# Kernel tuning notes

Hardware: AMD Instinct MI355X
Metric: run time of the kernel (lower is better)

The kernel has to match this reference:

```python
import jax, jax.numpy as jnp
import numpy as np

B, N, D, J, L = 8, 2046, 128, 128, 2  # batch, ops, feature len, jobs, blocks
C = N + 2  # ops + appended begin/end rows


def setup_inputs() -> dict:
    key = jax.random.key(0)
    ks = jax.random.split(key, 40)

    def w(k, shape, fan_in):
        return jax.random.normal(k, shape, jnp.float32) / np.float32(np.sqrt(fan_in))

    inp = {}
    inp["operation_features"] = jax.random.normal(ks[0], (B, N, D), jnp.float32)
    inp["same_type_mask"] = (jax.random.uniform(ks[1], (B, N, N)) > 0.5).astype(jnp.float32)
    inp["relations"] = jax.random.randint(ks[2], (B, N, 2), 0, N, jnp.int32)
    inp["begins_idx"] = jax.random.randint(ks[3], (B, J), 0, N, jnp.int32)
    inp["ends_idx"] = jax.random.randint(ks[4], (B, J), 0, N, jnp.int32)
    # begin_end_init params
    inp["init_bp_w"] = w(ks[5], (D, D), D); inp["init_bp_b"] = jnp.zeros((D,), jnp.float32)
    inp["init_ep_w"] = w(ks[6], (D, D), D); inp["init_ep_b"] = jnp.zeros((D,), jnp.float32)
    # per-block params, stacked on leading L axis
    inp["be_bp_w"] = w(ks[7], (L, D, D), D); inp["be_bp_b"] = jnp.zeros((L, D), jnp.float32)
    inp["be_ep_w"] = w(ks[8], (L, D, D), D); inp["be_ep_b"] = jnp.zeros((L, D), jnp.float32)
    inp["seq_mix_w"] = w(ks[9], (L, 3 * D, D), 3 * D); inp["seq_mix_b"] = jnp.zeros((L, D), jnp.float32)
    inp["attn_w_w"] = w(ks[10], (L, D, 3 * D), D); inp["attn_w_b"] = jnp.zeros((L, 3 * D), jnp.float32)
    inp["score_w"] = w(ks[11], (L, 2 * D), 2 * D); inp["score_b"] = jnp.zeros((L,), jnp.float32)
    inp["attn_out_w"] = w(ks[12], (L, D, D), D); inp["attn_out_b"] = jnp.zeros((L, D), jnp.float32)
    inp["mix_w"] = w(ks[13], (L, 2 * D, D), 2 * D); inp["mix_b"] = jnp.zeros((L, D), jnp.float32)
    return inp


def _begin_end(ops, begins_idx, ends_idx, bp_w, bp_b, ep_w, ep_b):
    gb = jnp.take_along_axis(ops, begins_idx[..., None], axis=1)  # [B,J,D]
    ge = jnp.take_along_axis(ops, ends_idx[..., None], axis=1)
    begin = jnp.mean(gb @ bp_w + bp_b, axis=1)  # [B,D]
    end = jnp.mean(ge @ ep_w + ep_b, axis=1)
    return begin, end


def _forward(operation_features, same_type_mask,
             init_bp_w, init_bp_b, init_ep_w, init_ep_b,
             be_bp_w, be_bp_b, be_ep_w, be_ep_b,
             seq_mix_w, seq_mix_b, attn_w_w, attn_w_b,
             score_w, score_b, attn_out_w, attn_out_b,
             mix_w, mix_b, relations, begins_idx, ends_idx):
    begin, end = _begin_end(operation_features, begins_idx, ends_idx,
                            init_bp_w, init_bp_b, init_ep_w, init_ep_b)
    feats = jnp.concatenate([operation_features, begin[:, None], end[:, None]], axis=1)  # [B,C,D]
    # -1 sentinels point to appended begin/end rows
    rel_p = jnp.where(relations[..., 0] == -1, N, relations[..., 0])  # [B,N]
    rel_s = jnp.where(relations[..., 1] == -1, N + 1, relations[..., 1])
    mask = jnp.zeros((B, C, C), jnp.float32)
    mask = mask.at[:, :N, :N].set(same_type_mask)
    mask = mask.at[:, N, N].set(1.0).at[:, N + 1, N + 1].set(1.0)

    for l in range(L):
        # --- OperationTimeRelationEncoder ---
        pred = jnp.take_along_axis(feats, rel_p[..., None], axis=1)  # [B,N,D]
        succ = jnp.take_along_axis(feats, rel_s[..., None], axis=1)
        mixed = jnp.concatenate([feats[:, :N], pred, succ], axis=-1) @ seq_mix_w[l] + seq_mix_b[l]
        b2, e2 = _begin_end(feats, begins_idx, ends_idx,
                            be_bp_w[l], be_bp_b[l], be_ep_w[l], be_ep_b[l])
        seq_feats = jnp.concatenate([mixed, b2[:, None], e2[:, None]], axis=1)  # [B,C,D]
        # --- SelfAttention (GAT-style concat score) ---
        qkv = feats @ attn_w_w[l] + attn_w_b[l]
        q, k, v = jnp.split(qkv, 3, axis=-1)  # each [B,C,D]
        wq, wk = score_w[l][:D], score_w[l][D:]
        # score(concat(q_i, k_j)) = q_i.wq + k_j.wk + b, then LeakyReLU
        scores = jax.nn.leaky_relu((q @ wq)[:, :, None] + (k @ wk)[:, None, :] + score_b[l])  # [B,C,C]
        attn = jax.nn.softmax(scores * mask, axis=-1)
        weighted = jnp.einsum('bij,bjh->bih', attn, v)  # [B,C,D]
        attn_out = weighted @ attn_out_w[l] + attn_out_b[l]
        # --- block mix ---
        feats = jnp.concatenate([seq_feats, attn_out], axis=-1) @ mix_w[l] + mix_b[l]

    return jnp.mean(feats, axis=1), feats


def reference(operation_features, same_type_mask,
              init_bp_w, init_bp_b, init_ep_w, init_ep_b,
              be_bp_w, be_bp_b, be_ep_w, be_ep_b,
              seq_mix_w, seq_mix_b, attn_w_w, attn_w_b,
              score_w, score_b, attn_out_w, attn_out_b,
              mix_w, mix_b, relations, begins_idx, ends_idx):
    return _forward(operation_features, same_type_mask,
                    init_bp_w, init_bp_b, init_ep_w, init_ep_b,
                    be_bp_w, be_bp_b, be_ep_w, be_ep_b,
                    seq_mix_w, seq_mix_b, attn_w_w, attn_w_b,
                    score_w, score_b, attn_out_w, attn_out_b,
                    mix_w, mix_b, relations, begins_idx, ends_idx)
```

## Files before the change

### kernel.cpp

```cpp
#include <hip/hip_runtime.h>

constexpr int kB = 8;
constexpr int kN = 2046;
constexpr int kC = 2048;
constexpr int kD = 128;
constexpr int kJ = 128;
constexpr int kL = 2;

typedef short bfrag8 __attribute__((ext_vector_type(8)));
typedef float f32x4 __attribute__((ext_vector_type(4)));

__device__ __forceinline__ float bf2f(unsigned short h) {
  union { unsigned u; float f; } x; x.u = ((unsigned)h) << 16; return x.f;
}
__device__ __forceinline__ unsigned short f2bf(float f) {
  union { float f; unsigned u; } x; x.f = f;
  unsigned u = x.u;
  if ((u & 0x7fffffffu) > 0x7f800000u) return (unsigned short)((u >> 16) | 0x40);
  return (unsigned short)((u + 0x7fffu + ((u >> 16) & 1u)) >> 16);
}
__device__ __forceinline__ unsigned short f2bf_fast(float f) {
  union { float f; unsigned u; } x; x.f = f;
  return (unsigned short)((x.u + 0x7fffu + ((x.u >> 16) & 1u)) >> 16);
}
__device__ __forceinline__ void split2(float x, unsigned short& h, unsigned short& l) {
  unsigned short hh = f2bf_fast(x);
  h = hh;
  l = f2bf_fast(x - bf2f(hh));
}

struct Raw {
  const void *ops, *mask;
  const int *rel, *bidx, *eidx;
  const void *ibw, *ibb, *iew, *ieb;
  const void *bbw, *bbb, *bew, *beb;
  const void *sw, *sb;
  const void *aw, *ab;
  const void *scw, *scb;
  const void *aow, *aob;
  const void *mw, *mb;
};

__device__ __forceinline__ float rp(const void* p, size_t i, bool bf) {
  return bf ? bf2f(((const unsigned short*)p)[i]) : ((const float*)p)[i];
}

__device__ __forceinline__ bool sniff(const Raw& r) {
  const unsigned* x = (const unsigned*)r.ops;
  int lane = (int)(threadIdx.x & 63);
  int hits = 0;
  #pragma unroll
  for (int q = 0; q < 16; ++q) {
    unsigned w = x[q * 64 + lane];
    unsigned e0 = (w >> 7) & 0xFFu;
    hits += (e0 == 0u || (e0 >= 96u && e0 <= 134u)) ? 1 : 0;
  }
  #pragma unroll
  for (int o = 1; o < 64; o <<= 1) hits += __shfl_xor(hits, o);
  return hits >= 512;
}

constexpr size_t OF_FEATS = 0;
constexpr size_t OF_SEQ   = 2097152;
constexpr size_t OF_ATTN  = 4194304;
constexpr size_t OF_V     = 6291456;
constexpr size_t OF_SQ    = 8388608;
constexpr size_t OF_SK    = 8404992;
constexpr size_t OF_U     = 8421376;
constexpr size_t OF_PART  = 8422400;
constexpr size_t OF_BMIX  = 8423424;
constexpr size_t OF_WT    = 8423680;

constexpr int WT_SEQH = 0;
constexpr int WT_SEQL = 49152;
constexpr int WT_VH   = 98304;
constexpr int WT_VL   = 114688;
constexpr int WT_MIXH = 131072;
constexpr int WT_MIXL = 163840;
constexpr int WT_LS   = 196608;

constexpr int RP_CAST = 4092;
constexpr int RP_MASK = 8184;
constexpr int RP_WT   = 8824;
constexpr int RP_WF   = 9082;
constexpr int RP_UV   = 9084;
constexpr int RP_BE   = 9100;
constexpr int RP_TOT  = 9101;

__device__ __forceinline__ f32x4 mfma16(bfrag8 a, bfrag8 b, f32x4 c) {
  return __builtin_amdgcn_mfma_f32_16x16x32_bf16(a, b, c, 0, 0, 0);
}

__global__ __launch_bounds__(256) void k_prep(Raw r, float* __restrict__ feats,
                                              unsigned* __restrict__ bits32,
                                              unsigned short* __restrict__ wt,
                                              float* __restrict__ bmix,
                                              float* __restrict__ u2,
                                              float* __restrict__ part) {
  __shared__ __align__(16) char smem[4096];
  int bid = blockIdx.x, t = threadIdx.x;
  bool bf = sniff(r);

  if (bid < RP_CAST) {
    int idx = bid * 256 + t;
    int elem = idx * 2;
    int b = elem / (kN * kD);
    int rr = elem - b * (kN * kD);
    float2 f;
    if (bf) {
      unsigned u = ((const unsigned*)r.ops)[idx];
      f.x = bf2f((unsigned short)(u & 0xffffu));
      f.y = bf2f((unsigned short)(u >> 16));
    } else {
      f = ((const float2*)r.ops)[idx];
    }
    *(float2*)(feats + (size_t)b * kC * kD + rr) = f;
  } else if (bid < RP_MASK) {
    int wave = t >> 6, lane = t & 63;
    int rr = (bid - RP_CAST) * 4 + wave;
    int b = rr / kN, i = rr - b * kN;
    unsigned chunk = 0;
    int je0 = lane * 32;
    if (bf) {
      const unsigned short* mrow = (const unsigned short*)r.mask + (size_t)rr * kN;
      if (je0 + 32 <= kN) {
        const unsigned* p32 = (const unsigned*)mrow;
        #pragma unroll
        for (int g = 0; g < 16; ++g) {
          unsigned v = p32[lane * 16 + g];
          if (v & 0xFFFFu) chunk |= 1u << (g * 2);
          if (v >> 16)     chunk |= 1u << (g * 2 + 1);
        }
      } else {
        for (int jj = je0; jj < kN; ++jj)
          if (mrow[jj] != 0) chunk |= 1u << (jj - je0);
      }
    } else {
      const unsigned* mrow = (const unsigned*)r.mask + (size_t)rr * kN;
      if (je0 + 32 <= kN) {
        const uint2* p64 = (const uint2*)mrow;
        #pragma unroll
        for (int g = 0; g < 16; ++g) {
          uint2 v = p64[lane * 16 + g];
          if (v.x) chunk |= 1u << (g * 2);
          if (v.y) chunk |= 1u << (g * 2 + 1);
        }
      } else {
        for (int jj = je0; jj < kN; ++jj)
          if (mrow[jj] != 0) chunk |= 1u << (jj - je0);
      }
    }
    bits32[((size_t)b * kC + i) * 64 + lane] = chunk;
  } else if (bid < RP_WT) {
    int idx = (bid - RP_MASK) * 256 + t;
    int l = idx / 81920;
    int rr = idx - l * 81920;
    const void* src; size_t si; int dH, dL, k, n;
    if (rr < 49152) {
      k = rr >> 7; n = rr & 127;
      src = r.sw; si = (size_t)l * 49152 + (size_t)k * 128 + n;
      dH = l * WT_LS + WT_SEQH; dL = l * WT_LS + WT_SEQL;
    } else if (rr < 65536) {
      int e = rr - 49152; k = e >> 7; n = e & 127;
      src = r.aw; si = (size_t)l * 49152 + (size_t)k * 384 + 256 + n;
      dH = l * WT_LS + WT_VH; dL = l * WT_LS + WT_VL;
    } else {
      int e = rr - 65536; k = e >> 7; n = e & 127;
      src = r.mw; si = (size_t)l * 32768 + (size_t)k * 128 + n;
      dH = l * WT_LS + WT_MIXH; dL = l * WT_LS + WT_MIXL;
    }
    float v = rp(src, si, bf);
    unsigned short h, lo;
    split2(v, h, lo);
    int kc = k >> 5, q = (k >> 3) & 3, e8 = k & 7;
    int fa = ((kc * 8 + (n >> 4)) * 64 + (q * 16 + (n & 15))) * 8 + e8;
    wt[dH + fa] = h;
    wt[dL + fa] = lo;
  } else if (bid < RP_WF) {
    int rb = bid - RP_WT;
    int l = rb / 129, d1 = rb - l * 129;
    if (t < 128) {
      int d = t;
      size_t mixbot = (size_t)l * 32768 + 16384;
      if (d1 < 128) {
        float acc = 0.f;
        for (int d2 = 0; d2 < kD; ++d2)
          acc += rp(r.aow, (size_t)l * 16384 + (size_t)d1 * 128 + d2, bf)
               * rp(r.mw, mixbot + (size_t)d2 * 128 + d, bf);
        unsigned short h, lo;
        split2(acc, h, lo);
        int k = 128 + d1;
        int kc = k >> 5, q = (k >> 3) & 3, e8 = k & 7;
        int fa = ((kc * 8 + (d >> 4)) * 64 + (q * 16 + (d & 15))) * 8 + e8;
        wt[l * WT_LS + WT_MIXH + fa] = h;
        wt[l * WT_LS + WT_MIXL + fa] = lo;
      } else {
        float acc = rp(r.mb, (size_t)l * 128 + d, bf);
        for (int d2 = 0; d2 < kD; ++d2)
          acc += rp(r.aob, (size_t)l * 128 + d2, bf)
               * rp(r.mw, mixbot + (size_t)d2 * 128 + d, bf);
        bmix[(size_t)l * kD + d] = acc;
      }
    }
  } else if (bid < RP_UV) {
    int l = bid - RP_WF;
    float* swm = (float*)smem;
    float* red = (float*)smem + 256;
    if (t < 128) {
      swm[t]       = rp(r.scw, (size_t)l * 256 + t, bf);
      swm[128 + t] = rp(r.scw, (size_t)l * 256 + 128 + t, bf);
    }
    __syncthreads();
    if (t < 128) {
      int k = t;
      size_t base = (size_t)l * 49152 + (size_t)k * 384;
      float uq = 0.f, uk = 0.f;
      for (int d2 = 0; d2 < kD; ++d2) {
        uq += rp(r.aw, base + d2, bf) * swm[d2];
        uk += rp(r.aw, base + 128 + d2, bf) * swm[128 + d2];
      }
      float* u = u2 + (size_t)l * 272;
      u[k] = uq; u[128 + k] = uk;
      red[k] = rp(r.ab, (size_t)l * 384 + k, bf) * swm[k]
             + rp(r.ab, (size_t)l * 384 + 128 + k, bf) * swm[128 + k];
    }
    __syncthreads();
    if (t == 0) {
      float s = rp(r.scb, l, bf);
      for (int i = 0; i < 128; ++i) s += red[i];
      u2[(size_t)l * 272 + 256] = s;
    }
  } else if (bid < RP_BE) {
    int rb = bid - RP_UV;
    int b = rb >> 1, sel = rb & 1;
    float* msh = (float*)smem;
    const int* idx = (sel ? r.eidx : r.bidx) + b * kJ;
    const void* wv = sel ? r.iew : r.ibw;
    const void* bb = sel ? r.ieb : r.ibb;
    if (t < 128) {
      int d = t;
      float acc = 0.f;
      for (int j = 0; j < kJ; ++j)
        acc += rp(r.ops, ((size_t)b * kN + idx[j]) * kD + d, bf);
      msh[d] = acc * (1.0f / kJ);
    }
    __syncthreads();
    if (t < 128) {
      int d = t;
      float o = rp(bb, d, bf);
      for (int k = 0; k < kD; ++k) o += msh[k] * rp(wv, (size_t)k * kD + d, bf);
      feats[(size_t)b * kC * kD + (size_t)(kN + sel) * kD + d] = o;
    }
  } else {
    #pragma unroll
    for (int q = 0; q < 4; ++q) part[q * 256 + t] = 0.f;
  }
}

__global__ __launch_bounds__(256) void k_stage1(Raw r, int l,
    const float* __restrict__ feats, const unsigned short* __restrict__ wt,
    const float* __restrict__ u2, float* __restrict__ seq,
    unsigned short* __restrict__ Vt, float* __restrict__ sq, float* __restrict__ sk)
{
  __shared__ __align__(16) char smem[21504];
  unsigned short (*Ah)[64 * 40] = (unsigned short(*)[64 * 40])smem;
  unsigned short (*Al)[64 * 40] = (unsigned short(*)[64 * 40])(smem + 10240);
  float* su = (float*)(smem + 20480);
  int bid = blockIdx.x, t = threadIdx.x;
  int lane = t & 63, w = t >> 6, m = lane & 15, quad = lane >> 4;
  bool bf = sniff(r);
  const unsigned short* wl = wt + (size_t)l * WT_LS;

  if (bid < 512) {
    bool isv = bid >= 256;
    int rb = isv ? bid - 256 : bid;
    int gr0 = rb * 64;
    int b = gr0 >> 11, r0 = gr0 & 2047;
    int arow = t >> 2, kq = (t & 3) * 8;
    int nl = r0 + arow;
    const float* fb = feats + (size_t)b * kC * kD;
    const float *s0, *s1, *s2;
    if (!isv) {
      int nr = (nl <= kN - 1) ? nl : (kN - 1);
      const int* rel = r.rel + ((size_t)b * kN + nr) * 2;
      int rpd = rel[0], rsc = rel[1];
      int p = (rpd < 0) ? kN : rpd;
      int s = (rsc < 0) ? (kN + 1) : rsc;
      s0 = fb + (size_t)nl * kD;
      s1 = fb + (size_t)p * kD;
      s2 = fb + (size_t)s * kD;
    } else {
      s0 = fb + (size_t)nl * kD; s1 = s0; s2 = s0;
      su[t] = u2[(size_t)l * 272 + t];
    }
    const int K = isv ? 128 : 384;
    const unsigned short* wth = isv ? (wl + WT_VH) : (wl + WT_SEQH);
    const unsigned short* wtl = isv ? (wl + WT_VL) : (wl + WT_SEQL);
    const unsigned short* pbh = wth + (size_t)(w * 2) * 512 + lane * 8;
    const unsigned short* pbl = wtl + (size_t)(w * 2) * 512 + lane * 8;
    float pq = 0.f, pk2 = 0.f;

    auto build = [&](int kb, int buf) {
      int kg = kb + kq;
      const float* sp;
      if (!isv) sp = (kg < 128) ? (s0 + kg) : (kg < 256) ? (s1 + kg - 128) : (s2 + kg - 256);
      else      sp = s0 + kg;
      float4 xa = *(const float4*)sp;
      float4 xb = *(const float4*)(sp + 4);
      if (isv) {
        pq  += xa.x * su[kg]     + xa.y * su[kg + 1] + xa.z * su[kg + 2] + xa.w * su[kg + 3]
             + xb.x * su[kg + 4] + xb.y * su[kg + 5] + xb.z * su[kg + 6] + xb.w * su[kg + 7];
        pk2 += xa.x * su[128 + kg]     + xa.y * su[128 + kg + 1] + xa.z * su[128 + kg + 2] + xa.w * su[128 + kg + 3]
             + xb.x * su[128 + kg + 4] + xb.y * su[128 + kg + 5] + xb.z * su[128 + kg + 6] + xb.w * su[128 + kg + 7];
      }
      unsigned short h[8], lo[8];
      split2(xa.x, h[0], lo[0]); split2(xa.y, h[1], lo[1]);
      split2(xa.z, h[2], lo[2]); split2(xa.w, h[3], lo[3]);
      split2(xb.x, h[4], lo[4]); split2(xb.y, h[5], lo[5]);
      split2(xb.z, h[6], lo[6]); split2(xb.w, h[7], lo[7]);
      uint4 ph, pl;
      ph.x = h[0] | ((unsigned)h[1] << 16);  ph.y = h[2] | ((unsigned)h[3] << 16);
      ph.z = h[4] | ((unsigned)h[5] << 16);  ph.w = h[6] | ((unsigned)h[7] << 16);
      pl.x = lo[0] | ((unsigned)lo[1] << 16); pl.y = lo[2] | ((unsigned)lo[3] << 16);
      pl.z = lo[4] | ((unsigned)lo[5] << 16); pl.w = lo[6] | ((unsigned)lo[7] << 16);
      *(uint4*)&Ah[buf][arow * 40 + kq] = ph;
      *(uint4*)&Al[buf][arow * 40 + kq] = pl;
    };

    f32x4 acc[4][2];
    #pragma unroll
    for (int mi = 0; mi < 4; ++mi) { acc[mi][0] = {0.f,0.f,0.f,0.f}; acc[mi][1] = {0.f,0.f,0.f,0.f}; }

    __syncthreads();
    build(0, 0);
    __syncthreads();
    for (int kb = 0; kb < K; kb += 32) {
      int cur = (kb >> 5) & 1;
      int kc = kb >> 5;
      bfrag8 bh0 = *(const bfrag8*)(pbh + (size_t)kc * 4096);
      bfrag8 bh1 = *(const bfrag8*)(pbh + (size_t)kc * 4096 + 512);
      bfrag8 bl0 = {}, bl1 = {};
      if (!bf) {
        bl0 = *(const bfrag8*)(pbl + (size_t)kc * 4096);
        bl1 = *(const bfrag8*)(pbl + (size_t)kc * 4096 + 512);
      }
      if (kb + 32 < K) build(kb + 32, cur ^ 1);
      #pragma unroll
      for (int mi = 0; mi < 4; ++mi) {
        bfrag8 ah = *(const bfrag8*)&Ah[cur][(mi * 16 + m) * 40 + quad * 8];
        bfrag8 al = *(const bfrag8*)&Al[cur][(mi * 16 + m) * 40 + quad * 8];
        acc[mi][0] = mfma16(ah, bh0, acc[mi][0]);
        acc[mi][0] = mfma16(al, bh0, acc[mi][0]);
        acc[mi][1] = mfma16(ah, bh1, acc[mi][1]);
        acc[mi][1] = mfma16(al, bh1, acc[mi][1]);
        if (!bf) {
          acc[mi][0] = mfma16(ah, bl0, acc[mi][0]);
          acc[mi][1] = mfma16(ah, bl1, acc[mi][1]);
        }
      }
      __syncthreads();
    }

    int n0 = w * 32 + m;
    if (!isv) {
      float bv0 = rp(r.sb, (size_t)l * 128 + n0, bf);
      float bv1 = rp(r.sb, (size_t)l * 128 + n0 + 16, bf);
      #pragma unroll
      for (int mi = 0; mi < 4; ++mi)
        #pragma unroll
        for (int reg = 0; reg < 4; ++reg) {
          int ra = r0 + mi * 16 + quad * 4 + reg;
          if (ra < kN) {
            seq[((size_t)b * kC + ra) * kD + n0]      = acc[mi][0][reg] + bv0;
            seq[((size_t)b * kC + ra) * kD + n0 + 16] = acc[mi][1][reg] + bv1;
          }
        }
    } else {
      float bv0 = rp(r.ab, (size_t)l * 384 + 256 + n0, bf);
      float bv1 = rp(r.ab, (size_t)l * 384 + 256 + n0 + 16, bf);
      unsigned short* vtb = Vt + (size_t)b * 262144;
      #pragma unroll
      for (int mi = 0; mi < 4; ++mi)
        #pragma unroll
        for (int reg = 0; reg < 4; ++reg) {
          int c = r0 + mi * 16 + quad * 4 + reg;
          int kc = c >> 5, cq = (c >> 3) & 3, e8 = c & 7;
          int lp = cq * 16 + m;
          vtb[((kc * 8 + w * 2) * 64 + lp) * 8 + e8]       = f2bf_fast(acc[mi][0][reg] + bv0);
          vtb[((kc * 8 + w * 2 + 1) * 64 + lp) * 8 + e8]   = f2bf_fast(acc[mi][1][reg] + bv1);
        }
      pq  += __shfl_xor(pq, 1);  pq  += __shfl_xor(pq, 2);
      pk2 += __shfl_xor(pk2, 1); pk2 += __shfl_xor(pk2, 2);
      if ((t & 3) == 0) {
        sq[(size_t)b * kC + nl] = pq + u2[(size_t)l * 272 + 256];
        sk[(size_t)b * kC + nl] = pk2;
      }
    }
  } else {
    int rb = bid - 512;
    int b = rb >> 1, sel = rb & 1;
    float* msh = (float*)smem;
    const int* idx = (sel ? r.eidx : r.bidx) + b * kJ;
    const void* wv = sel ? r.bew : r.bbw;
    const void* bb = sel ? r.beb : r.bbb;
    size_t wbase = (size_t)l * kD * kD, bbase = (size_t)l * kD;
    if (t < 128) {
      int d = t;
      const float* fb2 = feats + (size_t)b * kC * kD;
      float acc = 0.f;
      for (int j = 0; j < kJ; ++j) acc += fb2[(size_t)idx[j] * kD + d];
      msh[d] = acc * (1.0f / kJ);
    }
    __syncthreads();
    if (t < 128) {
      int d = t;
      float o = rp(bb, bbase + d, bf);
      for (int k = 0; k < kD; ++k) o += msh[k] * rp(wv, wbase + (size_t)k * kD + d, bf);
      seq[(size_t)b * kC * kD + (size_t)(kN + sel) * kD + d] = o;
    }
  }
}

__global__ __launch_bounds__(256) void k_attn_pv_mfma(
    const unsigned* __restrict__ bits,
    const float* __restrict__ sq, const float* __restrict__ sk,
    const unsigned short* __restrict__ Vt,
    float* __restrict__ outw)
{
  int b = blockIdx.y;
  int i0 = blockIdx.x * 32;
  int t = threadIdx.x, lane = t & 63, w = t >> 6;

  __shared__ unsigned short pshare[2][1024];
  __shared__ float sklds[kC];
  __shared__ unsigned bitlds[2048];
  __shared__ float ssq[32], smx[32], szv[32];

  const float* skb = sk + (size_t)b * kC;
  #pragma unroll
  for (int q = 0; q < 8; ++q) sklds[q * 256 + t] = skb[q * 256 + t];
  const unsigned* bitrow = bits + ((size_t)b * kC + i0) * 64;
  #pragma unroll
  for (int q = 0; q < 8; ++q) bitlds[q * 256 + t] = bitrow[q * 256 + t];
  if (t < 32) ssq[t] = sq[(size_t)b * kC + i0 + t];
  __syncthreads();

  {
    int rr = t >> 3, seg = t & 7;
    int ig = i0 + rr;
    bool ok = (ig < kN);
    float sqi2 = ssq[rr];
    const unsigned* bw = bitlds + rr * 64 + seg * 8;
    const float* sks = sklds + seg * 256;
    float mx;
    if (ok) {
      float msk = -3e38f;
      #pragma unroll 1
      for (int w8 = 0; w8 < 8; ++w8) {
        unsigned bb = bw[w8];
        #pragma unroll
        for (int q4 = 0; q4 < 8; ++q4) {
          float4 skv = *(const float4*)(sks + w8 * 32 + q4 * 4);
          unsigned nib = bb >> (q4 * 4);
          msk = (nib & 1u) ? fmaxf(msk, skv.x) : msk;
          msk = (nib & 2u) ? fmaxf(msk, skv.y) : msk;
          msk = (nib & 4u) ? fmaxf(msk, skv.z) : msk;
          msk = (nib & 8u) ? fmaxf(msk, skv.w) : msk;
        }
      }
      #pragma unroll
      for (int d2 = 1; d2 < 8; d2 <<= 1) msk = fmaxf(msk, __shfl_xor(msk, d2));
      float s = sqi2 + msk;
      mx = fmaxf(0.f, fmaxf(s, 0.01f * s));
    } else {
      float s = sqi2 + sklds[ig & (kC - 1)];
      mx = fmaxf(0.f, fmaxf(s, 0.01f * s));
    }
    float emx = __expf(-mx);
    float zs = 0.f;
    if (ok) {
      #pragma unroll 1
      for (int w8 = 0; w8 < 8; ++w8) {
        unsigned bb = bw[w8];
        #pragma unroll
        for (int q4 = 0; q4 < 8; ++q4) {
          float4 skv = *(const float4*)(sks + w8 * 32 + q4 * 4);
          unsigned nib = bb >> (q4 * 4);
          float s1 = sqi2 + skv.x, l1 = fmaxf(s1, 0.01f * s1);
          float s2 = sqi2 + skv.y, l2 = fmaxf(s2, 0.01f * s2);
          float s3 = sqi2 + skv.z, l3 = fmaxf(s3, 0.01f * s3);
          float s4 = sqi2 + skv.w, l4 = fmaxf(s4, 0.01f * s4);
          zs += (nib & 1u) ? __expf(l1 - mx) : emx;
          zs += (nib & 2u) ? __expf(l2 - mx) : emx;
          zs += (nib & 4u) ? __expf(l3 - mx) : emx;
          zs += (nib & 8u) ? __expf(l4 - mx) : emx;
        }
      }
    } else {
      zs = 256.f * emx;
      if ((ig >> 8) == seg) {
        float s = sqi2 + sklds[ig & (kC - 1)];
        float lr = fmaxf(s, 0.01f * s);
        zs += __expf(lr - mx) - emx;
      }
    }
    #pragma unroll
    for (int d2 = 1; d2 < 8; d2 <<= 1) zs += __shfl_xor(zs, d2);
    if (seg == 0) { smx[rr] = mx; szv[rr] = 1.0f / zs; }
  }
  __syncthreads();

  int f = t >> 1, h = t & 1;
  int mt_b = f >> 6;
  int lb = f & 63;
  int irow_l = mt_b * 16 + (lb & 15);
  int quad_b = lb >> 4;
  int i_g = i0 + irow_l;
  float sqi = ssq[irow_l];
  float mri = smx[irow_l];
  int joff = quad_b * 8 + h * 4;
  bool irow_ok = (i_g < kN);
  const unsigned char* bitb = (const unsigned char*)bitlds + irow_l * 256;

  auto buildP = [&](int k0, int buf) {
    float4 skv = *(const float4*)(sklds + k0 + joff);
    unsigned byte;
    if (irow_ok) {
      byte = bitb[(k0 >> 3) + quad_b];
    } else {
      int d0 = i_g - (k0 + quad_b * 8);
      byte = ((unsigned)d0 < 8u) ? (1u << d0) : 0u;
    }
    unsigned nib = byte >> (h * 4);
    unsigned short us[4];
    float sv[4] = {skv.x, skv.y, skv.z, skv.w};
    #pragma unroll
    for (int dj = 0; dj < 4; ++dj) {
      float s = sqi + sv[dj];
      float lr = fmaxf(s, 0.01f * s);
      float val = ((nib >> dj) & 1u) ? lr : 0.f;
      us[dj] = f2bf_fast(__expf(val - mri));
    }
    uint2 pk;
    pk.x = us[0] | ((unsigned)us[1] << 16);
    pk.y = us[2] | ((unsigned)us[3] << 16);
    *(uint2*)(&pshare[buf][f * 8 + h * 4]) = pk;
  };

  f32x4 acc00 = {0.f, 0.f, 0.f, 0.f}, acc01 = acc00, acc10 = acc00, acc11 = acc00;
  int m = lane & 15, quad = lane >> 4;
  int nbase = w * 32;
  const unsigned short* vtb = Vt + (size_t)b * 262144;
  const unsigned short* p0 = vtb + (size_t)(w * 2) * 512 + lane * 8;
  const unsigned short* p1 = p0 + 512;

  buildP(0, 0);
  bfrag8 b0n = *(const bfrag8*)p0;
  bfrag8 b1n = *(const bfrag8*)p1;
  __syncthreads();

  for (int k0 = 0; k0 < kC; k0 += 32) {
    int cur = (k0 >> 5) & 1;
    bfrag8 bf0 = b0n, bf1 = b1n;
    if (k0 + 32 < kC) {
      size_t off = (size_t)((k0 >> 5) + 1) * 4096;
      b0n = *(const bfrag8*)(p0 + off);
      b1n = *(const bfrag8*)(p1 + off);
    }
    bfrag8 a0 = *(const bfrag8*)(&pshare[cur][(0 * 64 + lane) * 8]);
    bfrag8 a1 = *(const bfrag8*)(&pshare[cur][(1 * 64 + lane) * 8]);
    acc00 = mfma16(a0, bf0, acc00);
    acc01 = mfma16(a0, bf1, acc01);
    acc10 = mfma16(a1, bf0, acc10);
    acc11 = mfma16(a1, bf1, acc11);
    if (k0 + 32 < kC) buildP(k0 + 32, cur ^ 1);
    __syncthreads();
  }

  #pragma unroll
  for (int reg = 0; reg < 4; ++reg) {
    int il_a = quad * 4 + reg;
    int i_a = i0 + il_a;
    int i_b = i_a + 16;
    float za = szv[il_a];
    float zb = szv[il_a + 16];
    float* oa = outw + ((size_t)b * kC + i_a) * kD + nbase + m;
    float* ob = outw + ((size_t)b * kC + i_b) * kD + nbase + m;
    oa[0]  = acc00[reg] * za;
    oa[16] = acc01[reg] * za;
    ob[0]  = acc10[reg] * zb;
    ob[16] = acc11[reg] * zb;
  }
}

__global__ __launch_bounds__(256) void k_mix64(Raw r, int l,
    const float* __restrict__ seqb, const float* __restrict__ attnw,
    const unsigned short* __restrict__ wt, const float* __restrict__ bmix,
    float* __restrict__ featsOut, void* __restrict__ outx, float* __restrict__ part,
    int mode)
{
  __shared__ __align__(16) char smem[20480];
  unsigned short (*Ah)[64 * 40] = (unsigned short(*)[64 * 40])smem;
  unsigned short (*Al)[64 * 40] = (unsigned short(*)[64 * 40])(smem + 10240);
  constexpr int K = 256;
  int bid = blockIdx.x, t = threadIdx.x;
  int lane = t & 63, w = t >> 6, m = lane & 15, quad = lane >> 4;
  bool bf = sniff(r);
  int gr0 = bid * 64;
  int b = gr0 >> 11;
  int arow = t >> 2, kq = (t & 3) * 8;
  const float* s0 = seqb  + (size_t)(gr0 + arow) * kD;
  const float* s1 = attnw + (size_t)(gr0 + arow) * kD;
  const unsigned short* wth = wt + (size_t)l * WT_LS + WT_MIXH;
  const unsigned short* wtl = wt + (size_t)l * WT_LS + WT_MIXL;
  const unsigned short* pbh = wth + (size_t)(w * 2) * 512 + lane * 8;
  const unsigned short* pbl = wtl + (size_t)(w * 2) * 512 + lane * 8;

  auto build = [&](int kb, int buf) {
    int kg = kb + kq;
    const float* sp = (kg < kD) ? (s0 + kg) : (s1 + kg - kD);
    float4 xa = *(const float4*)sp;
    float4 xb = *(const float4*)(sp + 4);
    unsigned short h[8], lo[8];
    split2(xa.x, h[0], lo[0]); split2(xa.y, h[1], lo[1]);
    split2(xa.z, h[2], lo[2]); split2(xa.w, h[3], lo[3]);
    split2(xb.x, h[4], lo[4]); split2(xb.y, h[5], lo[5]);
    split2(xb.z, h[6], lo[6]); split2(xb.w, h[7], lo[7]);
    uint4 ph, pl;
    ph.x = h[0] | ((unsigned)h[1] << 16);  ph.y = h[2] | ((unsigned)h[3] << 16);
    ph.z = h[4] | ((unsigned)h[5] << 16);  ph.w = h[6] | ((unsigned)h[7] << 16);
    pl.x = lo[0] | ((unsigned)lo[1] << 16); pl.y = lo[2] | ((unsigned)lo[3] << 16);
    pl.z = lo[4] | ((unsigned)lo[5] << 16); pl.w = lo[6] | ((unsigned)lo[7] << 16);
    *(uint4*)&Ah[buf][arow * 40 + kq] = ph;
    *(uint4*)&Al[buf][arow * 40 + kq] = pl;
  };

  f32x4 acc[4][2];
  #pragma unroll
  for (int mi = 0; mi < 4; ++mi) { acc[mi][0] = {0.f,0.f,0.f,0.f}; acc[mi][1] = {0.f,0.f,0.f,0.f}; }

  build(0, 0);
  __syncthreads();
  for (int kb = 0; kb < K; kb += 32) {
    int cur = (kb >> 5) & 1;
    int kc = kb >> 5;
    bfrag8 bh0 = *(const bfrag8*)(pbh + (size_t)kc * 4096);
    bfrag8 bh1 = *(const bfrag8*)(pbh + (size_t)kc * 4096 + 512);
    bfrag8 bl0 = {}, bl1 = {};
    if (!bf) {
      bl0 = *(const bfrag8*)(pbl + (size_t)kc * 4096);
      bl1 = *(const bfrag8*)(pbl + (size_t)kc * 4096 + 512);
    }
    if (kb + 32 < K) build(kb + 32, cur ^ 1);
    #pragma unroll
    for (int mi = 0; mi < 4; ++mi) {
      bfrag8 ah = *(const bfrag8*)&Ah[cur][(mi * 16 + m) * 40 + quad * 8];
      bfrag8 al = *(const bfrag8*)&Al[cur][(mi * 16 + m) * 40 + quad * 8];
      acc[mi][0] = mfma16(ah, bh0, acc[mi][0]);
      acc[mi][0] = mfma16(al, bh0, acc[mi][0]);
      acc[mi][1] = mfma16(ah, bh1, acc[mi][1]);
      acc[mi][1] = mfma16(al, bh1, acc[mi][1]);
      if (!bf) {
        acc[mi][0] = mfma16(ah, bl0, acc[mi][0]);
        acc[mi][1] = mfma16(ah, bl1, acc[mi][1]);
      }
    }
    __syncthreads();
  }

  int n0 = w * 32 + m;
  float bv0 = bmix[(size_t)l * kD + n0];
  float bv1 = bmix[(size_t)l * kD + n0 + 16];
  if (mode == 0) {
    #pragma unroll
    for (int mi = 0; mi < 4; ++mi)
      #pragma unroll
      for (int reg = 0; reg < 4; ++reg) {
        size_t row = (size_t)gr0 + mi * 16 + quad * 4 + reg;
        featsOut[row * kD + n0]      = acc[mi][0][reg] + bv0;
        featsOut[row * kD + n0 + 16] = acc[mi][1][reg] + bv1;
      }
  } else {
    float sum0 = 0.f, sum1 = 0.f;
    #pragma unroll
    for (int mi = 0; mi < 4; ++mi)
      #pragma unroll
      for (int reg = 0; reg < 4; ++reg) {
        size_t row = (size_t)gr0 + mi * 16 + quad * 4 + reg;
        float v0 = acc[mi][0][reg] + bv0;
        float v1 = acc[mi][1][reg] + bv1;
        if (bf) {
          unsigned short* o = (unsigned short*)outx + 1024;
          o[row * kD + n0]      = f2bf(v0);
          o[row * kD + n0 + 16] = f2bf(v1);
        } else {
          float* o = (float*)outx + 1024;
          o[row * kD + n0]      = v0;
          o[row * kD + n0 + 16] = v1;
        }
        sum0 += v0; sum1 += v1;
      }
    sum0 += __shfl_xor(sum0, 16); sum0 += __shfl_xor(sum0, 32);
    sum1 += __shfl_xor(sum1, 16); sum1 += __shfl_xor(sum1, 32);
    if (quad == 0) {
      atomicAdd(&part[(size_t)b * kD + n0],      sum0);
      atomicAdd(&part[(size_t)b * kD + n0 + 16], sum1);
    }
  }
}

__global__ __launch_bounds__(128) void k_mean(Raw r, const float* __restrict__ part,
                                              void* __restrict__ out) {
  bool bf = sniff(r);
  int b = blockIdx.x, d = threadIdx.x;
  float v = part[(size_t)b * kD + d] * (1.0f / kC);
  if (bf) ((unsigned short*)out)[b * kD + d] = f2bf(v);
  else    ((float*)out)[b * kD + d] = v;
}

extern "C" void kernel_launch(void* const* d_in, const int* in_sizes, int n_in,
                              void* d_out, int out_size, void* d_ws, size_t ws_size,
                              hipStream_t stream) {
  Raw r;
  r.ops = d_in[0];  r.mask = d_in[1];
  r.rel = (const int*)d_in[2]; r.bidx = (const int*)d_in[3]; r.eidx = (const int*)d_in[4];
  r.ibw = d_in[5];  r.ibb = d_in[6];  r.iew = d_in[7];  r.ieb = d_in[8];
  r.bbw = d_in[9];  r.bbb = d_in[10]; r.bew = d_in[11]; r.beb = d_in[12];
  r.sw  = d_in[13]; r.sb  = d_in[14]; r.aw  = d_in[15]; r.ab  = d_in[16];
  r.scw = d_in[17]; r.scb = d_in[18]; r.aow = d_in[19]; r.aob = d_in[20];
  r.mw  = d_in[21]; r.mb  = d_in[22];

  float* ws    = (float*)d_ws;
  float* feats = ws + OF_FEATS;
  float* seq   = ws + OF_SEQ;
  float* attnw = ws + OF_ATTN;
  float* sq    = ws + OF_SQ;
  float* sk    = ws + OF_SK;
  float* u2    = ws + OF_U;
  float* part  = ws + OF_PART;
  float* bmix  = ws + OF_BMIX;
  unsigned short* wt = (unsigned short*)(ws + OF_WT);
  unsigned short* Vt = (unsigned short*)(ws + OF_V);
  unsigned*     bits = (unsigned*)(ws + OF_V + 1048576);

  k_prep<<<RP_TOT, 256, 0, stream>>>(r, feats, bits, wt, bmix, u2, part);

  for (int l = 0; l < kL; ++l) {
    k_stage1<<<528, 256, 0, stream>>>(r, l, feats, wt, u2, seq, Vt, sq, sk);
    k_attn_pv_mfma<<<dim3(64, kB), 256, 0, stream>>>(bits, sq, sk, Vt, attnw);
    k_mix64<<<256, 256, 0, stream>>>(r, l, seq, attnw, wt, bmix, feats, d_out, part,
                                     (l == kL - 1) ? 1 : 0);
  }

  k_mean<<<kB, 128, 0, stream>>>(r, part, d_out);
}
```

Baseline: 459.7 us.

## Store intermediates as pre-split bf16 hi/lo pairs and ballot-pack mask bits

Intermediate activations (feats, seq, attention output) are now stored as pre-split bf16 hi/lo arrays rather than fp32. Consumers can copy them straight into LDS for the MFMA split-precision GEMMs instead of re-splitting on every load. The producer kernels do the split once at write time. Separately, the mask-to-bitmask pass uses wave ballots over coalesced loads in place of strided per-lane loops, at the cost of extra ballots and a bit-spread step.

```diff
diff --git a/kernel.cpp b/kernel.cpp
--- a/kernel.cpp
+++ b/kernel.cpp
@@ -27,6 +27,14 @@
   unsigned short hh = f2bf_fast(x);
   h = hh;
   l = f2bf_fast(x - bf2f(hh));
+}
+__device__ __forceinline__ unsigned spread16(unsigned x) {
+  x &= 0xFFFFu;
+  x = (x | (x << 8)) & 0x00FF00FFu;
+  x = (x | (x << 4)) & 0x0F0F0F0Fu;
+  x = (x | (x << 2)) & 0x33333333u;
+  x = (x | (x << 1)) & 0x55555555u;
+  return x;
 }
 
 struct Raw {
@@ -60,16 +68,19 @@
   return hits >= 512;
 }
 
-constexpr size_t OF_FEATS = 0;
-constexpr size_t OF_SEQ   = 2097152;
-constexpr size_t OF_ATTN  = 4194304;
-constexpr size_t OF_V     = 6291456;
-constexpr size_t OF_SQ    = 8388608;
-constexpr size_t OF_SK    = 8404992;
-constexpr size_t OF_U     = 8421376;
-constexpr size_t OF_PART  = 8422400;
-constexpr size_t OF_BMIX  = 8423424;
-constexpr size_t OF_WT    = 8423680;
+constexpr size_t OF_FHI = 0;
+constexpr size_t OF_FLO = 1048576;
+constexpr size_t OF_SHI = 2097152;
+constexpr size_t OF_SLO = 3145728;
+constexpr size_t OF_AHI = 4194304;
+constexpr size_t OF_ALO = 5242880;
+constexpr size_t OF_V   = 6291456;
+constexpr size_t OF_SQ  = 8388608;
+constexpr size_t OF_SK  = 8404992;
+constexpr size_t OF_U   = 8421376;
+constexpr size_t OF_PART= 8422400;
+constexpr size_t OF_BMIX= 8423424;
+constexpr size_t OF_WT  = 8423680;
 
 constexpr int WT_SEQH = 0;
 constexpr int WT_SEQL = 49152;
@@ -91,7 +102,9 @@
   return __builtin_amdgcn_mfma_f32_16x16x32_bf16(a, b, c, 0, 0, 0);
 }
 
-__global__ __launch_bounds__(256) void k_prep(Raw r, float* __restrict__ feats,
+__global__ __launch_bounds__(256) void k_prep(Raw r,
+                                              unsigned short* __restrict__ fhi,
+                                              unsigned short* __restrict__ flo,
                                               unsigned* __restrict__ bits32,
                                               unsigned short* __restrict__ wt,
                                               float* __restrict__ bmix,
@@ -106,51 +119,56 @@
     int elem = idx * 2;
     int b = elem / (kN * kD);
     int rr = elem - b * (kN * kD);
-    float2 f;
+    unsigned uh, ul;
     if (bf) {
-      unsigned u = ((const unsigned*)r.ops)[idx];
-      f.x = bf2f((unsigned short)(u & 0xffffu));
-      f.y = bf2f((unsigned short)(u >> 16));
+      uh = ((const unsigned*)r.ops)[idx];
+      ul = 0u;
     } else {
-      f = ((const float2*)r.ops)[idx];
-    }
-    *(float2*)(feats + (size_t)b * kC * kD + rr) = f;
+      float2 f = ((const float2*)r.ops)[idx];
+      unsigned short h0, l0, h1, l1;
+      split2(f.x, h0, l0); split2(f.y, h1, l1);
+      uh = (unsigned)h0 | ((unsigned)h1 << 16);
+      ul = (unsigned)l0 | ((unsigned)l1 << 16);
+    }
+    size_t wi = ((size_t)b * kC * kD + rr) >> 1;
+    ((unsigned*)fhi)[wi] = uh;
+    ((unsigned*)flo)[wi] = ul;
   } else if (bid < RP_MASK) {
     int wave = t >> 6, lane = t & 63;
     int rr = (bid - RP_CAST) * 4 + wave;
     int b = rr / kN, i = rr - b * kN;
-    unsigned chunk = 0;
-    int je0 = lane * 32;
+    unsigned word;
     if (bf) {
-      const unsigned short* mrow = (const unsigned short*)r.mask + (size_t)rr * kN;
-      if (je0 + 32 <= kN) {
-        const unsigned* p32 = (const unsigned*)mrow;
-        #pragma unroll
-        for (int g = 0; g < 16; ++g) {
-          unsigned v = p32[lane * 16 + g];
-          if (v & 0xFFFFu) chunk |= 1u << (g * 2);
-          if (v >> 16)     chunk |= 1u << (g * 2 + 1);
-        }
-      } else {
-        for (int jj = je0; jj < kN; ++jj)
-          if (mrow[jj] != 0) chunk |= 1u << (jj - je0);
-      }
+      const unsigned* p32 = (const unsigned*)((const unsigned short*)r.mask + (size_t)rr * kN);
+      unsigned long long s0 = 0, s1 = 0;
+      int myg = lane >> 2;
+      #pragma unroll
+      for (int g = 0; g < 16; ++g) {
+        int widx = g * 64 + lane;
+        if (widx > 1022) widx = 1022;
+        unsigned v = p32[widx];
+        unsigned long long b0 = __ballot((v & 0xFFFFu) != 0u);
+        unsigned long long b1 = __ballot((v >> 16) != 0u);
+        if (g == myg) { s0 = b0; s1 = b1; }
+      }
+      int wsub = lane & 3;
+      word = spread16((unsigned)(s0 >> (16 * wsub)))
+           | (spread16((unsigned)(s1 >> (16 * wsub))) << 1);
     } else {
-      const unsigned* mrow = (const unsigned*)r.mask + (size_t)rr * kN;
-      if (je0 + 32 <= kN) {
-        const uint2* p64 = (const uint2*)mrow;
-        #pragma unroll
-        for (int g = 0; g < 16; ++g) {
-          uint2 v = p64[lane * 16 + g];
-          if (v.x) chunk |= 1u << (g * 2);
-          if (v.y) chunk |= 1u << (g * 2 + 1);
-        }
-      } else {
-        for (int jj = je0; jj < kN; ++jj)
-          if (mrow[jj] != 0) chunk |= 1u << (jj - je0);
-      }
-    }
-    bits32[((size_t)b * kC + i) * 64 + lane] = chunk;
+      const unsigned* p32 = (const unsigned*)r.mask + (size_t)rr * kN;
+      unsigned long long sb = 0;
+      int myg = lane >> 1;
+      #pragma unroll
+      for (int g = 0; g < 32; ++g) {
+        int widx = g * 64 + lane;
+        if (widx > 2045) widx = 2045;
+        unsigned long long bal = __ballot(p32[widx] != 0u);
+        if (g == myg) sb = bal;
+      }
+      word = (unsigned)(sb >> (32 * (lane & 1)));
+    }
+    if (lane == 63) word &= 0x3FFFFFFFu;
+    bits32[((size_t)b * kC + i) * 64 + lane] = word;
   } else if (bid < RP_WT) {
     int idx = (bid - RP_MASK) * 256 + t;
     int l = idx / 81920;
@@ -249,7 +267,10 @@
       int d = t;
       float o = rp(bb, d, bf);
       for (int k = 0; k < kD; ++k) o += msh[k] * rp(wv, (size_t)k * kD + d, bf);
-      feats[(size_t)b * kC * kD + (size_t)(kN + sel) * kD + d] = o;
+      unsigned short hh, ll;
+      split2(o, hh, ll);
+      size_t ri = ((size_t)b * kC + kN + sel) * kD + d;
+      fhi[ri] = hh; flo[ri] = ll;
     }
   } else {
     #pragma unroll
@@ -258,8 +279,10 @@
 }
 
 __global__ __launch_bounds__(256) void k_stage1(Raw r, int l,
-    const float* __restrict__ feats, const unsigned short* __restrict__ wt,
-    const float* __restrict__ u2, float* __restrict__ seq,
+    const unsigned short* __restrict__ fhi, const unsigned short* __restrict__ flo,
+    const unsigned short* __restrict__ wt,
+    const float* __restrict__ u2,
+    unsigned short* __restrict__ shi, unsigned short* __restrict__ slo,
     unsigned short* __restrict__ Vt, float* __restrict__ sq, float* __restrict__ sk)
 {
   __shared__ __align__(16) char smem[21504];
@@ -278,20 +301,23 @@
     int b = gr0 >> 11, r0 = gr0 & 2047;
     int arow = t >> 2, kq = (t & 3) * 8;
     int nl = r0 + arow;
-    const float* fb = feats + (size_t)b * kC * kD;
-    const float *s0, *s1, *s2;
-    if (!isv) {
-      int nr = (nl <= kN - 1) ? nl : (kN - 1);
-      const int* rel = r.rel + ((size_t)b * kN + nr) * 2;
-      int rpd = rel[0], rsc = rel[1];
-      int p = (rpd < 0) ? kN : rpd;
-      int s = (rsc < 0) ? (kN + 1) : rsc;
-      s0 = fb + (size_t)nl * kD;
-      s1 = fb + (size_t)p * kD;
-      s2 = fb + (size_t)s * kD;
-    } else {
-      s0 = fb + (size_t)nl * kD; s1 = s0; s2 = s0;
-      su[t] = u2[(size_t)l * 272 + t];
+    const unsigned short *h0, *h1, *h2, *lo0, *lo1, *lo2;
+    {
+      size_t base = (size_t)b * kC;
+      if (!isv) {
+        int nr = (nl <= kN - 1) ? nl : (kN - 1);
+        const int* rel = r.rel + ((size_t)b * kN + nr) * 2;
+        int rpd = rel[0], rsc = rel[1];
+        int p = (rpd < 0) ? kN : rpd;
+        int s = (rsc < 0) ? (kN + 1) : rsc;
+        h0 = fhi + (base + nl) * kD; lo0 = flo + (base + nl) * kD;
+        h1 = fhi + (base + p) * kD;  lo1 = flo + (base + p) * kD;
+        h2 = fhi + (base + s) * kD;  lo2 = flo + (base + s) * kD;
+      } else {
+        h0 = fhi + (base + nl) * kD; lo0 = flo + (base + nl) * kD;
+        h1 = h0; h2 = h0; lo1 = lo0; lo2 = lo0;
+        su[t] = u2[(size_t)l * 272 + t];
+      }
     }
     const int K = isv ? 128 : 384;
     const unsigned short* wth = isv ? (wl + WT_VH) : (wl + WT_SEQH);
@@ -302,29 +328,26 @@
 
     auto build = [&](int kb, int buf) {
       int kg = kb + kq;
-      const float* sp;
-      if (!isv) sp = (kg < 128) ? (s0 + kg) : (kg < 256) ? (s1 + kg - 128) : (s2 + kg - 256);
-      else      sp = s0 + kg;
-      float4 xa = *(const float4*)sp;
-      float4 xb = *(const float4*)(sp + 4);
+      const unsigned short *hp, *lp;
+      if (!isv) {
+        if (kg < 128)      { hp = h0 + kg;       lp = lo0 + kg; }
+        else if (kg < 256) { hp = h1 + kg - 128; lp = lo1 + kg - 128; }
+        else               { hp = h2 + kg - 256; lp = lo2 + kg - 256; }
+      } else { hp = h0 + kg; lp = lo0 + kg; }
+      uint4 hv = *(const uint4*)hp;
+      uint4 lv = *(const uint4*)lp;
       if (isv) {
-        pq  += xa.x * su[kg]     + xa.y * su[kg + 1] + xa.z * su[kg + 2] + xa.w * su[kg + 3]
-             + xb.x * su[kg + 4] + xb.y * su[kg + 5] + xb.z * su[kg + 6] + xb.w * su[kg + 7];
-        pk2 += xa.x * su[128 + kg]     + xa.y * su[128 + kg + 1] + xa.z * su[128 + kg + 2] + xa.w * su[128 + kg + 3]
-             + xb.x * su[128 + kg + 4] + xb.y * su[128 + kg + 5] + xb.z * su[128 + kg + 6] + xb.w * su[128 + kg + 7];
-      }
-      unsigned short h[8], lo[8];
-      split2(xa.x, h[0], lo[0]); split2(xa.y, h[1], lo[1]);
-      split2(xa.z, h[2], lo[2]); split2(xa.w, h[3], lo[3]);
-      split2(xb.x, h[4], lo[4]); split2(xb.y, h[5], lo[5]);
-      split2(xb.z, h[6], lo[6]); split2(xb.w, h[7], lo[7]);
-      uint4 ph, pl;
-      ph.x = h[0] | ((unsigned)h[1] << 16);  ph.y = h[2] | ((unsigned)h[3] << 16);
-      ph.z = h[4] | ((unsigned)h[5] << 16);  ph.w = h[6] | ((unsigned)h[7] << 16);
-      pl.x = lo[0] | ((unsigned)lo[1] << 16); pl.y = lo[2] | ((unsigned)lo[3] << 16);
-      pl.z = lo[4] | ((unsigned)lo[5] << 16); pl.w = lo[6] | ((unsigned)lo[7] << 16);
-      *(uint4*)&Ah[buf][arow * 40 + kq] = ph;
-      *(uint4*)&Al[buf][arow * 40 + kq] = pl;
+        const unsigned short* hs = (const unsigned short*)&hv;
+        const unsigned short* ls = (const unsigned short*)&lv;
+        #pragma unroll
+        for (int j = 0; j < 8; ++j) {
+          float x = bf2f(hs[j]) + bf2f(ls[j]);
+          pq  += x * su[kg + j];
+          pk2 += x * su[128 + kg + j];
+        }
+      }
+      *(uint4*)&Ah[buf][arow * 40 + kq] = hv;
+      *(uint4*)&Al[buf][arow * 40 + kq] = lv;
     };
 
     f32x4 acc[4][2];
@@ -371,8 +394,12 @@
         for (int reg = 0; reg < 4; ++reg) {
           int ra = r0 + mi * 16 + quad * 4 + reg;
           if (ra < kN) {
-            seq[((size_t)b * kC + ra) * kD + n0]      = acc[mi][0][reg] + bv0;
-            seq[((size_t)b * kC + ra) * kD + n0 + 16] = acc[mi][1][reg] + bv1;
+            size_t ri = ((size_t)b * kC + ra) * kD;
+            unsigned short hh, ll;
+            split2(acc[mi][0][reg] + bv0, hh, ll);
+            shi[ri + n0] = hh; slo[ri + n0] = ll;
+            split2(acc[mi][1][reg] + bv1, hh, ll);
+            shi[ri + n0 + 16] = hh; slo[ri + n0 + 16] = ll;
           }
         }
     } else {
@@ -406,9 +433,12 @@
     size_t wbase = (size_t)l * kD * kD, bbase = (size_t)l * kD;
     if (t < 128) {
       int d = t;
-      const float* fb2 = feats + (size_t)b * kC * kD;
+      size_t base = (size_t)b * kC * kD;
       float acc = 0.f;
-      for (int j = 0; j < kJ; ++j) acc += fb2[(size_t)idx[j] * kD + d];
+      for (int j = 0; j < kJ; ++j) {
+        size_t ri = base + (size_t)idx[j] * kD + d;
+        acc += bf2f(fhi[ri]) + bf2f(flo[ri]);
+      }
       msh[d] = acc * (1.0f / kJ);
     }
     __syncthreads();
@@ -416,7 +446,10 @@
       int d = t;
       float o = rp(bb, bbase + d, bf);
       for (int k = 0; k < kD; ++k) o += msh[k] * rp(wv, wbase + (size_t)k * kD + d, bf);
-      seq[(size_t)b * kC * kD + (size_t)(kN + sel) * kD + d] = o;
+      unsigned short hh, ll;
+      split2(o, hh, ll);
+      size_t ri = ((size_t)b * kC + kN + sel) * kD + d;
+      shi[ri] = hh; slo[ri] = ll;
     }
   }
 }
@@ -425,7 +458,7 @@
     const unsigned* __restrict__ bits,
     const float* __restrict__ sq, const float* __restrict__ sk,
     const unsigned short* __restrict__ Vt,
-    float* __restrict__ outw)
+    unsigned short* __restrict__ ahi, unsigned short* __restrict__ alo)
 {
   int b = blockIdx.y;
   int i0 = blockIdx.x * 32;
@@ -584,19 +617,22 @@
     int i_b = i_a + 16;
     float za = szv[il_a];
     float zb = szv[il_a + 16];
-    float* oa = outw + ((size_t)b * kC + i_a) * kD + nbase + m;
-    float* ob = outw + ((size_t)b * kC + i_b) * kD + nbase + m;
-    oa[0]  = acc00[reg] * za;
-    oa[16] = acc01[reg] * za;
-    ob[0]  = acc10[reg] * zb;
-    ob[16] = acc11[reg] * zb;
+    size_t ra = ((size_t)b * kC + i_a) * kD + nbase + m;
+    size_t rb2 = ((size_t)b * kC + i_b) * kD + nbase + m;
+    unsigned short hh, ll;
+    split2(acc00[reg] * za, hh, ll); ahi[ra] = hh;       alo[ra] = ll;
+    split2(acc01[reg] * za, hh, ll); ahi[ra + 16] = hh;  alo[ra + 16] = ll;
+    split2(acc10[reg] * zb, hh, ll); ahi[rb2] = hh;      alo[rb2] = ll;
+    split2(acc11[reg] * zb, hh, ll); ahi[rb2 + 16] = hh; alo[rb2 + 16] = ll;
   }
 }
 
 __global__ __launch_bounds__(256) void k_mix64(Raw r, int l,
-    const float* __restrict__ seqb, const float* __restrict__ attnw,
+    const unsigned short* __restrict__ shi, const unsigned short* __restrict__ slo,
+    const unsigned short* __restrict__ ahi, const unsigned short* __restrict__ alo,
     const unsigned short* __restrict__ wt, const float* __restrict__ bmix,
-    float* __restrict__ featsOut, void* __restrict__ outx, float* __restrict__ part,
+    unsigned short* __restrict__ fhi, unsigned short* __restrict__ flo,
+    void* __restrict__ outx, float* __restrict__ part,
     int mode)
 {
   __shared__ __align__(16) char smem[20480];
@@ -609,8 +645,10 @@
   int gr0 = bid * 64;
   int b = gr0 >> 11;
   int arow = t >> 2, kq = (t & 3) * 8;
-  const float* s0 = seqb  + (size_t)(gr0 + arow) * kD;
-  const float* s1 = attnw + (size_t)(gr0 + arow) * kD;
+  const unsigned short* sh0 = shi + (size_t)(gr0 + arow) * kD;
+  const unsigned short* sl0 = slo + (size_t)(gr0 + arow) * kD;
+  const unsigned short* ah0 = ahi + (size_t)(gr0 + arow) * kD;
+  const unsigned short* al0 = alo + (size_t)(gr0 + arow) * kD;
   const unsigned short* wth = wt + (size_t)l * WT_LS + WT_MIXH;
   const unsigned short* wtl = wt + (size_t)l * WT_LS + WT_MIXL;
   const unsigned short* pbh = wth + (size_t)(w * 2) * 512 + lane * 8;
@@ -618,21 +656,11 @@
 
   auto build = [&](int kb, int buf) {
     int kg = kb + kq;
-    const float* sp = (kg < kD) ? (s0 + kg) : (s1 + kg - kD);
-    float4 xa = *(const float4*)sp;
-    float4 xb = *(const float4*)(sp + 4);
-    unsigned short h[8], lo[8];
-    split2(xa.x, h[0], lo[0]); split2(xa.y, h[1], lo[1]);
-    split2(xa.z, h[2], lo[2]); split2(xa.w, h[3], lo[3]);
-    split2(xb.x, h[4], lo[4]); split2(xb.y, h[5], lo[5]);
-    split2(xb.z, h[6], lo[6]); split2(xb.w, h[7], lo[7]);
-    uint4 ph, pl;
-    ph.x = h[0] | ((unsigned)h[1] << 16);  ph.y = h[2] | ((unsigned)h[3] << 16);
-    ph.z = h[4] | ((unsigned)h[5] << 16);  ph.w = h[6] | ((unsigned)h[7] << 16);
-    pl.x = lo[0] | ((unsigned)lo[1] << 16); pl.y = lo[2] | ((unsigned)lo[3] << 16);
-    pl.z = lo[4] | ((unsigned)lo[5] << 16); pl.w = lo[6] | ((unsigned)lo[7] << 16);
-    *(uint4*)&Ah[buf][arow * 40 + kq] = ph;
-    *(uint4*)&Al[buf][arow * 40 + kq] = pl;
+    const unsigned short *hp, *lp;
+    if (kg < kD) { hp = sh0 + kg;       lp = sl0 + kg; }
+    else         { hp = ah0 + kg - kD;  lp = al0 + kg - kD; }
+    *(uint4*)&Ah[buf][arow * 40 + kq] = *(const uint4*)hp;
+    *(uint4*)&Al[buf][arow * 40 + kq] = *(const uint4*)lp;
   };
 
   f32x4 acc[4][2];
@@ -676,9 +704,12 @@
     for (int mi = 0; mi < 4; ++mi)
       #pragma unroll
       for (int reg = 0; reg < 4; ++reg) {
-        size_t row = (size_t)gr0 + mi * 16 + quad * 4 + reg;
-        featsOut[row * kD + n0]      = acc[mi][0][reg] + bv0;
-        featsOut[row * kD + n0 + 16] = acc[mi][1][reg] + bv1;
+        size_t row = ((size_t)gr0 + mi * 16 + quad * 4 + reg) * kD;
+        unsigned short hh, ll;
+        split2(acc[mi][0][reg] + bv0, hh, ll);
+        fhi[row + n0] = hh; flo[row + n0] = ll;
+        split2(acc[mi][1][reg] + bv1, hh, ll);
+        fhi[row + n0 + 16] = hh; flo[row + n0 + 16] = ll;
       }
   } else {
     float sum0 = 0.f, sum1 = 0.f;
@@ -730,26 +761,29 @@
   r.scw = d_in[17]; r.scb = d_in[18]; r.aow = d_in[19]; r.aob = d_in[20];
   r.mw  = d_in[21]; r.mb  = d_in[22];
 
-  float* ws    = (float*)d_ws;
-  float* feats = ws + OF_FEATS;
-  float* seq   = ws + OF_SEQ;
-  float* attnw = ws + OF_ATTN;
-  float* sq    = ws + OF_SQ;
-  float* sk    = ws + OF_SK;
-  float* u2    = ws + OF_U;
-  float* part  = ws + OF_PART;
-  float* bmix  = ws + OF_BMIX;
+  float* ws = (float*)d_ws;
+  unsigned short* fhi = (unsigned short*)(ws + OF_FHI);
+  unsigned short* flo = (unsigned short*)(ws + OF_FLO);
+  unsigned short* shi = (unsigned short*)(ws + OF_SHI);
+  unsigned short* slo = (unsigned short*)(ws + OF_SLO);
+  unsigned short* ahi = (unsigned short*)(ws + OF_AHI);
+  unsigned short* alo = (unsigned short*)(ws + OF_ALO);
+  unsigned short* Vt  = (unsigned short*)(ws + OF_V);
+  unsigned*      bits = (unsigned*)(ws + OF_V + 1048576);
+  float* sq   = ws + OF_SQ;
+  float* sk   = ws + OF_SK;
+  float* u2   = ws + OF_U;
+  float* part = ws + OF_PART;
+  float* bmix = ws + OF_BMIX;
   unsigned short* wt = (unsigned short*)(ws + OF_WT);
-  unsigned short* Vt = (unsigned short*)(ws + OF_V);
-  unsigned*     bits = (unsigned*)(ws + OF_V + 1048576);
-
-  k_prep<<<RP_TOT, 256, 0, stream>>>(r, feats, bits, wt, bmix, u2, part);
+
+  k_prep<<<RP_TOT, 256, 0, stream>>>(r, fhi, flo, bits, wt, bmix, u2, part);
 
   for (int l = 0; l < kL; ++l) {
-    k_stage1<<<528, 256, 0, stream>>>(r, l, feats, wt, u2, seq, Vt, sq, sk);
-    k_attn_pv_mfma<<<dim3(64, kB), 256, 0, stream>>>(bits, sq, sk, Vt, attnw);
-    k_mix64<<<256, 256, 0, stream>>>(r, l, seq, attnw, wt, bmix, feats, d_out, part,
-                                     (l == kL - 1) ? 1 : 0);
+    k_stage1<<<528, 256, 0, stream>>>(r, l, fhi, flo, wt, u2, shi, slo, Vt, sq, sk);
+    k_attn_pv_mfma<<<dim3(64, kB), 256, 0, stream>>>(bits, sq, sk, Vt, ahi, alo);
+    k_mix64<<<256, 256, 0, stream>>>(r, l, shi, slo, ahi, alo, wt, bmix, fhi, flo,
+                                     d_out, part, (l == kL - 1) ? 1 : 0);
   }
 
   k_mean<<<kB, 128, 0, stream>>>(r, part, d_out);
```

Result: slower. 471.9 us (+2.6%).
